# Optimization experiments

Hardware: AMD Instinct MI355X
Metric: run time of the kernel (lower is better)

The kernel has to match this reference:

```python
import jax, jax.numpy as jnp
import numpy as np

N_NODES = 50000
N_EDGES = 1500000
MEM_DIM = 128
EFEAT_DIM = 128
TEMP_DIM = 100


def setup_inputs() -> dict:
    key = jax.random.key(0)
    ks = jax.random.split(key, 10)
    src = jax.random.randint(ks[0], (N_EDGES,), 0, N_NODES)
    dst = jax.random.randint(ks[1], (N_EDGES,), 0, N_NODES)
    edge_ts = jax.random.uniform(ks[2], (N_EDGES,), dtype=jnp.float32) * 100.0
    edge_feats = jax.random.normal(ks[3], (N_EDGES, EFEAT_DIM), dtype=jnp.float32)
    mem_s = jax.random.normal(ks[4], (N_NODES, MEM_DIM), dtype=jnp.float32)
    last_update_t = jax.random.uniform(ks[5], (N_NODES,), dtype=jnp.float32) * 50.0
    # TimeEncode: deterministic init, w = 1/10**linspace(0,9,dim), bias zeros
    time_w = jnp.asarray(1.0 / 10 ** np.linspace(0, 9, TEMP_DIM), dtype=jnp.float32)
    time_b = jnp.zeros((TEMP_DIM,), dtype=jnp.float32)
    msg_dim = MEM_DIM + MEM_DIM + EFEAT_DIM + TEMP_DIM  # 484
    W_ih = jax.random.normal(ks[6], (3 * MEM_DIM, msg_dim), dtype=jnp.float32) * 0.05
    W_hh = jax.random.normal(ks[7], (3 * MEM_DIM, MEM_DIM), dtype=jnp.float32) * 0.05
    b_ih = jax.random.normal(ks[8], (3 * MEM_DIM,), dtype=jnp.float32) * 0.05
    b_hh = jax.random.normal(ks[9], (3 * MEM_DIM,), dtype=jnp.float32) * 0.05
    return {"src": src, "dst": dst, "edge_ts": edge_ts, "edge_feats": edge_feats,
            "mem_s": mem_s, "last_update_t": last_update_t,
            "time_w": time_w, "time_b": time_b,
            "W_ih": W_ih, "W_hh": W_hh, "b_ih": b_ih, "b_hh": b_hh}


def reference(src, dst, edge_ts, edge_feats, mem_s, last_update_t,
              time_w, time_b, W_ih, W_hh, b_ih, b_hh):
    N, H = mem_s.shape
    E = src.shape[0]
    # --- agg_last: per-dst node, pick the incoming edge with max timestamp ---
    max_ts = jax.ops.segment_max(edge_ts, dst, num_segments=N)  # -inf if no msgs
    is_max = edge_ts == max_ts[dst]
    eidx = jnp.arange(E)
    win = jax.ops.segment_max(jnp.where(is_max, eidx, -1), dst, num_segments=N)
    has_msg = win >= 0  # [N]
    w = jnp.clip(win, 0)  # safe index for empty nodes (masked later)
    # --- msg_fn_cat, computed only for the winning edge per node ---
    src_w = src[w]  # [N]
    delta = edge_ts[w] - last_update_t[src_w]  # [N]
    tenc = jnp.cos(delta[:, None] * time_w[None, :] + time_b[None, :])  # [N,T]
    # winning edge's dst == node itself, so edges.dst['s'] == mem_s
    m_bar = jnp.concatenate([mem_s[src_w], mem_s, edge_feats[w], tenc], axis=1)  # [N,484]
    # --- GRUCell(m_bar, mem_s) ---
    gi = m_bar @ W_ih.T + b_ih  # [N, 3H]
    gh = mem_s @ W_hh.T + b_hh  # [N, 3H]
    i_r, i_z, i_n = jnp.split(gi, 3, axis=1)
    h_r, h_z, h_n = jnp.split(gh, 3, axis=1)
    r = jax.nn.sigmoid(i_r + h_r)
    z = jax.nn.sigmoid(i_z + h_z)
    n = jnp.tanh(i_n + r * h_n)
    h_new = (1.0 - z) * n + z * mem_s
    # only nodes that received messages are updated by update_all
    s_out = jnp.where(has_msg[:, None], h_new, mem_s)
    ts_out = jnp.where(has_msg, max_ts, last_update_t)
    return s_out, ts_out
```

## Files before the change

### kernel.cpp

```cpp
#include <hip/hip_runtime.h>
#include <stdint.h>
#include <math.h>

#define N_NODES 50000
#define N_EDGES 1500000
#define HDIM 128
#define TDIM 100
#define KPAD 512
#define BM 64
#define NT 512
#define NBLOCKS ((N_NODES + BM - 1) / BM)

typedef __attribute__((ext_vector_type(8))) short short8v;
typedef __attribute__((ext_vector_type(4))) float f32x4;
typedef __attribute__((ext_vector_type(4))) unsigned int u32x4;

__device__ __forceinline__ unsigned short f2bf(float x) {
    unsigned int u = __float_as_uint(x);
    return (unsigned short)((u + 0x7fffu + ((u >> 16) & 1u)) >> 16);
}
__device__ __forceinline__ float sigmoidf_(float x) { return 1.0f / (1.0f + __expf(-x)); }
__device__ __forceinline__ float tanhf_(float x) { return 2.0f / (1.0f + __expf(-2.0f * x)) - 1.0f; }

__global__ void scan_edges_kernel(const int* __restrict__ dst,
                                  const float* __restrict__ edge_ts,
                                  unsigned long long* __restrict__ keys) {
    int e = blockIdx.x * 256 + threadIdx.x;
    if (e < N_EDGES) {
        unsigned tsb = __float_as_uint(__builtin_nontemporal_load(&edge_ts[e]));
        int d = __builtin_nontemporal_load(&dst[e]);
        unsigned cur_hi = ((const unsigned*)keys)[2 * d + 1];
        if (tsb >= cur_hi) {
            unsigned long long key =
                ((unsigned long long)tsb << 32) | (unsigned int)(e + 1);
            atomicMax(&keys[d], key);
        }
    }
}

__global__ void convert_w_kernel(const float* __restrict__ Wih, const float* __restrict__ Whh,
                                 unsigned short* __restrict__ wbF1, unsigned short* __restrict__ wbF2) {
    int t = blockIdx.x * 256 + threadIdx.x;
    if (t < 24576) {
        int b = t >> 10, kt = (t >> 6) & 15, l = t & 63;
        int g3 = b >> 3, nq = (b >> 1) & 3, nf = b & 1;
        int srow = g3 * 128 + nq * 32 + nf * 16 + (l & 15);
        int scol = kt * 32 + (l >> 4) * 8;
        unsigned short v[8];
        #pragma unroll
        for (int j = 0; j < 8; ++j)
            v[j] = (scol + j < 484) ? f2bf(Wih[srow * 484 + scol + j]) : (unsigned short)0;
        uint4 pk;
        pk.x = (unsigned)v[0] | ((unsigned)v[1] << 16);
        pk.y = (unsigned)v[2] | ((unsigned)v[3] << 16);
        pk.z = (unsigned)v[4] | ((unsigned)v[5] << 16);
        pk.w = (unsigned)v[6] | ((unsigned)v[7] << 16);
        *(uint4*)&wbF1[(size_t)t * 8] = pk;
    } else if (t < 24576 + 6144) {
        int t2 = t - 24576;
        int b = t2 >> 8, kt = (t2 >> 6) & 3, l = t2 & 63;
        int g3 = b >> 3, nq = (b >> 1) & 3, nf = b & 1;
        int srow = g3 * 128 + nq * 32 + nf * 16 + (l & 15);
        int scol = kt * 32 + (l >> 4) * 8;
        unsigned short v[8];
        #pragma unroll
        for (int j = 0; j < 8; ++j) v[j] = f2bf(Whh[srow * 128 + scol + j]);
        uint4 pk;
        pk.x = (unsigned)v[0] | ((unsigned)v[1] << 16);
        pk.y = (unsigned)v[2] | ((unsigned)v[3] << 16);
        pk.z = (unsigned)v[4] | ((unsigned)v[5] << 16);
        pk.w = (unsigned)v[6] | ((unsigned)v[7] << 16);
        *(uint4*)&wbF2[(size_t)t2 * 8] = pk;
    }
}

__global__ __launch_bounds__(NT, 4)
void gru_mfma_kernel(const int* __restrict__ src,
                     const float* __restrict__ edge_ts,
                     const float* __restrict__ ef,
                     const float* __restrict__ mem,
                     const float* __restrict__ lut,
                     const float* __restrict__ tw,
                     const float* __restrict__ tb,
                     const float* __restrict__ bih,
                     const float* __restrict__ bhh,
                     const unsigned short* __restrict__ wbF1,
                     const unsigned short* __restrict__ wbF2,
                     const unsigned long long* __restrict__ keys,
                     float* __restrict__ out) {
    __shared__ unsigned short Alds[BM * KPAD];
    const int tid = threadIdx.x;
    const int base = blockIdx.x * BM;

    {
        const int i = tid >> 3, l8 = tid & 7;
        const int n = base + i;
        if (n < N_NODES) {
            unsigned long long key = keys[n];
            const int has = (key != 0ULL);
            const int e = has ? (int)((unsigned)key - 1u) : 0;
            const int s = src[e];
            const float tv = edge_ts[e];
            const float d = tv - lut[s];
            if (l8 == 0)
                __builtin_nontemporal_store(has ? tv : lut[n],
                                            &out[(size_t)N_NODES * HDIM + n]);
            const int swg = i & 7;
            unsigned short* Arow = &Alds[i * KPAD];
            #pragma unroll
            for (int p = 0; p < 8; ++p) {
                const int gk = p * 8 + l8, k0 = gk * 8;
                float f[8];
                if (k0 < 384) {
                    const float* sp = (k0 < 128) ? mem + (size_t)s * HDIM + k0
                                    : (k0 < 256) ? mem + (size_t)n * HDIM + (k0 - 128)
                                                 : ef + (size_t)e * HDIM + (k0 - 256);
                    u32x4 w0 = __builtin_nontemporal_load((const u32x4*)sp);
                    u32x4 w1 = __builtin_nontemporal_load((const u32x4*)sp + 1);
                    f[0]=__uint_as_float(w0.x); f[1]=__uint_as_float(w0.y);
                    f[2]=__uint_as_float(w0.z); f[3]=__uint_as_float(w0.w);
                    f[4]=__uint_as_float(w1.x); f[5]=__uint_as_float(w1.y);
                    f[6]=__uint_as_float(w1.z); f[7]=__uint_as_float(w1.w);
                } else {
                    #pragma unroll
                    for (int j2 = 0; j2 < 8; ++j2) {
                        int q = k0 - 384 + j2;
                        f[j2] = (q < TDIM) ? cosf(fmaf(d, tw[q], tb[q])) : 0.f;
                    }
                }
                uint4 pk;
                pk.x = (unsigned)f2bf(f[0]) | ((unsigned)f2bf(f[1]) << 16);
                pk.y = (unsigned)f2bf(f[2]) | ((unsigned)f2bf(f[3]) << 16);
                pk.z = (unsigned)f2bf(f[4]) | ((unsigned)f2bf(f[5]) << 16);
                pk.w = (unsigned)f2bf(f[6]) | ((unsigned)f2bf(f[7]) << 16);
                *(uint4*)&Arow[(size_t)(gk ^ swg) * 8] = pk;
            }
        }
    }
    __syncthreads();

    const int w = tid >> 6, l = tid & 63;
    const int mh = w >> 2, nq = w & 3;
    const int lr = l & 15, lh = l >> 4;

    const short8v* Bv1 = (const short8v*)wbF1 + l;
    const short8v* Bv2 = (const short8v*)wbF2 + l;
    int bo1[6], bo2[6];
    #pragma unroll
    for (int f = 0; f < 6; ++f) {
        const int bidx = ((f >> 1) * 4 + nq) * 2 + (f & 1);
        bo1[f] = bidx * 16 * 64;
        bo2[f] = bidx * 4 * 64;
    }

    const f32x4 fzero = {0.f, 0.f, 0.f, 0.f};
    f32x4 acc[4][2][2];
    #pragma unroll
    for (int q = 0; q < 4; ++q)
        #pragma unroll
        for (int nf = 0; nf < 2; ++nf)
            #pragma unroll
            for (int mf = 0; mf < 2; ++mf) acc[q][nf][mf] = fzero;

    #pragma unroll 2
    for (int kt = 0; kt < 16; ++kt) {
        short8v b[6];
        #pragma unroll
        for (int f = 0; f < 6; ++f) b[f] = Bv1[bo1[f] + kt * 64];
        short8v a[2];
        #pragma unroll
        for (int mf = 0; mf < 2; ++mf) {
            const int row = mh * 32 + mf * 16 + lr;
            a[mf] = *(const short8v*)&Alds[row * KPAD + ((kt * 32 + lh * 8) ^ ((row & 7) << 3))];
        }
        #pragma unroll
        for (int f = 0; f < 6; ++f)
            #pragma unroll
            for (int mf = 0; mf < 2; ++mf)
                acc[f >> 1][f & 1][mf] = __builtin_amdgcn_mfma_f32_16x16x32_bf16(
                    a[mf], b[f], acc[f >> 1][f & 1][mf], 0, 0, 0);
    }
    #pragma unroll 2
    for (int kt = 0; kt < 4; ++kt) {
        short8v b[6];
        #pragma unroll
        for (int f = 0; f < 6; ++f) b[f] = Bv2[bo2[f] + kt * 64];
        short8v a[2];
        #pragma unroll
        for (int mf = 0; mf < 2; ++mf) {
            const int row = mh * 32 + mf * 16 + lr;
            a[mf] = *(const short8v*)&Alds[row * KPAD + (((128 + kt * 32) + lh * 8) ^ ((row & 7) << 3))];
        }
        #pragma unroll
        for (int f = 0; f < 6; ++f) {
            const int q = (f >> 1) < 2 ? (f >> 1) : 3;
            #pragma unroll
            for (int mf = 0; mf < 2; ++mf)
                acc[q][f & 1][mf] = __builtin_amdgcn_mfma_f32_16x16x32_bf16(
                    a[mf], b[f], acc[q][f & 1][mf], 0, 0, 0);
        }
    }

    float br[2], bz[2], bin[2], bhn[2];
    #pragma unroll
    for (int nf = 0; nf < 2; ++nf) {
        const int c = nq * 32 + nf * 16 + lr;
        br[nf] = bih[c] + bhh[c];
        bz[nf] = bih[HDIM + c] + bhh[HDIM + c];
        bin[nf] = bih[2 * HDIM + c];
        bhn[nf] = bhh[2 * HDIM + c];
    }
    #pragma unroll
    for (int mf = 0; mf < 2; ++mf)
        #pragma unroll
        for (int ii = 0; ii < 4; ++ii) {
            const int row = mh * 32 + mf * 16 + lh * 4 + ii;
            const int node = base + row;
            if (node >= N_NODES) continue;
            const bool has = keys[node] != 0ULL;
            #pragma unroll
            for (int nf = 0; nf < 2; ++nf) {
                const int c = nq * 32 + nf * 16 + lr;
                const float r = sigmoidf_(acc[0][nf][mf][ii] + br[nf]);
                const float z = sigmoidf_(acc[1][nf][mf][ii] + bz[nf]);
                const float ng = tanhf_(acc[2][nf][mf][ii] + bin[nf] +
                                        r * (acc[3][nf][mf][ii] + bhn[nf]));
                const float h = __builtin_nontemporal_load(&mem[(size_t)node * HDIM + c]);
                __builtin_nontemporal_store(has ? (1.f - z) * ng + z * h : h,
                                            &out[(size_t)node * HDIM + c]);
            }
        }
}

extern "C" void kernel_launch(void* const* d_in, const int* in_sizes, int n_in,
                              void* d_out, int out_size, void* d_ws, size_t ws_size,
                              hipStream_t stream) {
    const int* src       = (const int*)d_in[0];
    const int* dst       = (const int*)d_in[1];
    const float* edge_ts = (const float*)d_in[2];
    const float* ef      = (const float*)d_in[3];
    const float* mem     = (const float*)d_in[4];
    const float* lut     = (const float*)d_in[5];
    const float* tw      = (const float*)d_in[6];
    const float* tb      = (const float*)d_in[7];
    const float* Wih     = (const float*)d_in[8];
    const float* Whh     = (const float*)d_in[9];
    const float* bih     = (const float*)d_in[10];
    const float* bhh     = (const float*)d_in[11];
    float* out = (float*)d_out;

    char* ws = (char*)d_ws;
    unsigned long long* keys = (unsigned long long*)ws;
    unsigned short* wbF1 = (unsigned short*)(ws + 524288);
    unsigned short* wbF2 = (unsigned short*)(ws + 917504);

    hipMemsetAsync(keys, 0, (size_t)N_NODES * 8, stream);
    scan_edges_kernel<<<(N_EDGES + 255) / 256, 256, 0, stream>>>(dst, edge_ts, keys);
    convert_w_kernel<<<(24576 + 6144 + 255) / 256, 256, 0, stream>>>(Wih, Whh, wbF1, wbF2);
    gru_mfma_kernel<<<NBLOCKS, NT, 0, stream>>>(
        src, edge_ts, ef, mem, lut, tw, tb, bih, bhh, wbF1, wbF2, keys, out);
}
```

Baseline: 152.0 us.

## Remap GRU warps to full-row column strips and read hidden state from LDS

Each of the 8 warps now owns a 16-column strip across all 64 rows and the three gates. Per K step it loads 3 weight fragments from global instead of 6, and 4 A fragments from LDS instead of 2. The weight pre-conversion is relaid out to match. The epilogue takes the old hidden state from the bf16 copy already staged in LDS instead of reloading fp32 from global, which adds bf16 rounding to the z*h term. Nodes with no message are now skipped, and a full device-to-device memcpy of mem into the output runs beforehand to cover them. That copy adds a whole extra pass over the state for nodes that almost all receive messages.

Result: faster. 139.9 us (-7.9%).

```diff
diff --git a/kernel.cpp b/kernel.cpp
--- a/kernel.cpp
+++ b/kernel.cpp
@@ -18,6 +18,9 @@
 __device__ __forceinline__ unsigned short f2bf(float x) {
     unsigned int u = __float_as_uint(x);
     return (unsigned short)((u + 0x7fffu + ((u >> 16) & 1u)) >> 16);
+}
+__device__ __forceinline__ float bf2f(unsigned short b) {
+    return __uint_as_float((unsigned)b << 16);
 }
 __device__ __forceinline__ float sigmoidf_(float x) { return 1.0f / (1.0f + __expf(-x)); }
 __device__ __forceinline__ float tanhf_(float x) { return 2.0f / (1.0f + __expf(-2.0f * x)) - 1.0f; }
@@ -43,8 +46,8 @@
     int t = blockIdx.x * 256 + threadIdx.x;
     if (t < 24576) {
         int b = t >> 10, kt = (t >> 6) & 15, l = t & 63;
-        int g3 = b >> 3, nq = (b >> 1) & 3, nf = b & 1;
-        int srow = g3 * 128 + nq * 32 + nf * 16 + (l & 15);
+        int g3 = b >> 3, n8 = b & 7;
+        int srow = g3 * 128 + n8 * 16 + (l & 15);
         int scol = kt * 32 + (l >> 4) * 8;
         unsigned short v[8];
         #pragma unroll
@@ -59,8 +62,8 @@
     } else if (t < 24576 + 6144) {
         int t2 = t - 24576;
         int b = t2 >> 8, kt = (t2 >> 6) & 3, l = t2 & 63;
-        int g3 = b >> 3, nq = (b >> 1) & 3, nf = b & 1;
-        int srow = g3 * 128 + nq * 32 + nf * 16 + (l & 15);
+        int g3 = b >> 3, n8 = b & 7;
+        int srow = g3 * 128 + n8 * 16 + (l & 15);
         int scol = kt * 32 + (l >> 4) * 8;
         unsigned short v[8];
         #pragma unroll
@@ -89,6 +92,7 @@
                      const unsigned long long* __restrict__ keys,
                      float* __restrict__ out) {
     __shared__ unsigned short Alds[BM * KPAD];
+    __shared__ unsigned char sh_has[BM];
     const int tid = threadIdx.x;
     const int base = blockIdx.x * BM;
 
@@ -102,9 +106,11 @@
             const int s = src[e];
             const float tv = edge_ts[e];
             const float d = tv - lut[s];
-            if (l8 == 0)
+            if (l8 == 0) {
+                sh_has[i] = (unsigned char)has;
                 __builtin_nontemporal_store(has ? tv : lut[n],
                                             &out[(size_t)N_NODES * HDIM + n]);
+            }
             const int swg = i & 7;
             unsigned short* Arow = &Alds[i * KPAD];
             #pragma unroll
@@ -139,96 +145,81 @@
     }
     __syncthreads();
 
-    const int w = tid >> 6, l = tid & 63;
-    const int mh = w >> 2, nq = w & 3;
+    const int n8 = tid >> 6, l = tid & 63;
     const int lr = l & 15, lh = l >> 4;
 
     const short8v* Bv1 = (const short8v*)wbF1 + l;
     const short8v* Bv2 = (const short8v*)wbF2 + l;
-    int bo1[6], bo2[6];
-    #pragma unroll
-    for (int f = 0; f < 6; ++f) {
-        const int bidx = ((f >> 1) * 4 + nq) * 2 + (f & 1);
-        bo1[f] = bidx * 16 * 64;
-        bo2[f] = bidx * 4 * 64;
-    }
 
     const f32x4 fzero = {0.f, 0.f, 0.f, 0.f};
-    f32x4 acc[4][2][2];
+    f32x4 acc[4][4];
     #pragma unroll
     for (int q = 0; q < 4; ++q)
         #pragma unroll
-        for (int nf = 0; nf < 2; ++nf)
-            #pragma unroll
-            for (int mf = 0; mf < 2; ++mf) acc[q][nf][mf] = fzero;
+        for (int mf = 0; mf < 4; ++mf) acc[q][mf] = fzero;
 
     #pragma unroll 2
     for (int kt = 0; kt < 16; ++kt) {
-        short8v b[6];
-        #pragma unroll
-        for (int f = 0; f < 6; ++f) b[f] = Bv1[bo1[f] + kt * 64];
-        short8v a[2];
-        #pragma unroll
-        for (int mf = 0; mf < 2; ++mf) {
-            const int row = mh * 32 + mf * 16 + lr;
+        short8v b[3];
+        #pragma unroll
+        for (int g3 = 0; g3 < 3; ++g3)
+            b[g3] = Bv1[((g3 * 8 + n8) * 16 + kt) * 64];
+        short8v a[4];
+        #pragma unroll
+        for (int mf = 0; mf < 4; ++mf) {
+            const int row = mf * 16 + lr;
             a[mf] = *(const short8v*)&Alds[row * KPAD + ((kt * 32 + lh * 8) ^ ((row & 7) << 3))];
         }
         #pragma unroll
-        for (int f = 0; f < 6; ++f)
+        for (int g3 = 0; g3 < 3; ++g3)
             #pragma unroll
-            for (int mf = 0; mf < 2; ++mf)
-                acc[f >> 1][f & 1][mf] = __builtin_amdgcn_mfma_f32_16x16x32_bf16(
-                    a[mf], b[f], acc[f >> 1][f & 1][mf], 0, 0, 0);
+            for (int mf = 0; mf < 4; ++mf)
+                acc[g3][mf] = __builtin_amdgcn_mfma_f32_16x16x32_bf16(
+                    a[mf], b[g3], acc[g3][mf], 0, 0, 0);
     }
     #pragma unroll 2
     for (int kt = 0; kt < 4; ++kt) {
-        short8v b[6];
-        #pragma unroll
-        for (int f = 0; f < 6; ++f) b[f] = Bv2[bo2[f] + kt * 64];
-        short8v a[2];
-        #pragma unroll
-        for (int mf = 0; mf < 2; ++mf) {
-            const int row = mh * 32 + mf * 16 + lr;
+        short8v b[3];
+        #pragma unroll
+        for (int g3 = 0; g3 < 3; ++g3)
+            b[g3] = Bv2[((g3 * 8 + n8) * 4 + kt) * 64];
+        short8v a[4];
+        #pragma unroll
+        for (int mf = 0; mf < 4; ++mf) {
+            const int row = mf * 16 + lr;
             a[mf] = *(const short8v*)&Alds[row * KPAD + (((128 + kt * 32) + lh * 8) ^ ((row & 7) << 3))];
         }
         #pragma unroll
-        for (int f = 0; f < 6; ++f) {
-            const int q = (f >> 1) < 2 ? (f >> 1) : 3;
+        for (int g3 = 0; g3 < 3; ++g3) {
+            const int q = (g3 < 2) ? g3 : 3;
             #pragma unroll
-            for (int mf = 0; mf < 2; ++mf)
-                acc[q][f & 1][mf] = __builtin_amdgcn_mfma_f32_16x16x32_bf16(
-                    a[mf], b[f], acc[q][f & 1][mf], 0, 0, 0);
-        }
-    }
-
-    float br[2], bz[2], bin[2], bhn[2];
+            for (int mf = 0; mf < 4; ++mf)
+                acc[q][mf] = __builtin_amdgcn_mfma_f32_16x16x32_bf16(
+                    a[mf], b[g3], acc[q][mf], 0, 0, 0);
+        }
+    }
+
+    const int c = n8 * 16 + lr;
+    const float br = bih[c] + bhh[c];
+    const float bz = bih[HDIM + c] + bhh[HDIM + c];
+    const float bin = bih[2 * HDIM + c];
+    const float bhn = bhh[2 * HDIM + c];
+    const int hg = 16 + (c >> 3);
+    const int ho = c & 7;
     #pragma unroll
-    for (int nf = 0; nf < 2; ++nf) {
-        const int c = nq * 32 + nf * 16 + lr;
-        br[nf] = bih[c] + bhh[c];
-        bz[nf] = bih[HDIM + c] + bhh[HDIM + c];
-        bin[nf] = bih[2 * HDIM + c];
-        bhn[nf] = bhh[2 * HDIM + c];
-    }
-    #pragma unroll
-    for (int mf = 0; mf < 2; ++mf)
+    for (int mf = 0; mf < 4; ++mf)
         #pragma unroll
         for (int ii = 0; ii < 4; ++ii) {
-            const int row = mh * 32 + mf * 16 + lh * 4 + ii;
+            const int row = mf * 16 + lh * 4 + ii;
             const int node = base + row;
             if (node >= N_NODES) continue;
-            const bool has = keys[node] != 0ULL;
-            #pragma unroll
-            for (int nf = 0; nf < 2; ++nf) {
-                const int c = nq * 32 + nf * 16 + lr;
-                const float r = sigmoidf_(acc[0][nf][mf][ii] + br[nf]);
-                const float z = sigmoidf_(acc[1][nf][mf][ii] + bz[nf]);
-                const float ng = tanhf_(acc[2][nf][mf][ii] + bin[nf] +
-                                        r * (acc[3][nf][mf][ii] + bhn[nf]));
-                const float h = __builtin_nontemporal_load(&mem[(size_t)node * HDIM + c]);
-                __builtin_nontemporal_store(has ? (1.f - z) * ng + z * h : h,
-                                            &out[(size_t)node * HDIM + c]);
-            }
+            if (!sh_has[row]) continue;
+            const float r = sigmoidf_(acc[0][mf][ii] + br);
+            const float z = sigmoidf_(acc[1][mf][ii] + bz);
+            const float ng = tanhf_(acc[2][mf][ii] + bin + r * (acc[3][mf][ii] + bhn));
+            const float h = bf2f(Alds[row * KPAD + (hg ^ (row & 7)) * 8 + ho]);
+            __builtin_nontemporal_store((1.f - z) * ng + z * h,
+                                        &out[(size_t)node * HDIM + c]);
         }
 }
 
@@ -257,6 +248,8 @@
     hipMemsetAsync(keys, 0, (size_t)N_NODES * 8, stream);
     scan_edges_kernel<<<(N_EDGES + 255) / 256, 256, 0, stream>>>(dst, edge_ts, keys);
     convert_w_kernel<<<(24576 + 6144 + 255) / 256, 256, 0, stream>>>(Wih, Whh, wbF1, wbF2);
+    hipMemcpyAsync(out, mem, (size_t)N_NODES * HDIM * sizeof(float),
+                   hipMemcpyDeviceToDevice, stream);
     gru_mfma_kernel<<<NBLOCKS, NT, 0, stream>>>(
         src, edge_ts, ef, mem, lut, tw, tb, bih, bhh, wbF1, wbF2, keys, out);
 }
```
